# Kernel optimization log

Hardware: AMD Instinct MI355X
Metric: run time of the kernel (lower is better)

## Reference

```python
import jax, jax.numpy as jnp
import numpy as np

B, Q, E, NH, L, P = 8, 1024, 256, 8, 4, 4
DH = E // NH
SHAPES = np.array([[128, 128], [64, 64], [32, 32], [16, 16]], dtype=np.int64)
STARTS = np.concatenate([[0], np.cumsum(SHAPES.prod(1))[:-1]]).astype(np.int64)
S_TOTAL = int(SHAPES.prod(1).sum())
EPS = 1e-5


def setup_inputs() -> dict:
    key = jax.random.key(0)
    ks = iter(jax.random.split(key, 40))
    def rn(shp, s=0.02):
        return jax.random.normal(next(ks), shp, jnp.float32) * s
    return {
        "tgt": rn((B, Q, E), 1.0),
        "query_pos": rn((B, Q, E), 1.0),
        "reference_points": jax.random.uniform(next(ks), (B, Q, L, 2), jnp.float32),
        "src": rn((B, S_TOTAL, E), 1.0),
        "spatial_shapes": jnp.asarray(SHAPES),
        "level_start_index": jnp.asarray(STARTS),
        "in_proj_w": rn((3 * E, E)), "in_proj_b": jnp.zeros((3 * E,), jnp.float32),
        "out_proj_w": rn((E, E)), "out_proj_b": jnp.zeros((E,), jnp.float32),
        "norm1_g": jnp.ones((E,), jnp.float32), "norm1_b": jnp.zeros((E,), jnp.float32),
        "off_w": rn((NH * L * P * 2, E)), "off_b": rn((NH * L * P * 2,), 0.5),
        "aw_w": rn((NH * L * P, E)), "aw_b": jnp.zeros((NH * L * P,), jnp.float32),
        "vp_w": rn((E, E)), "vp_b": jnp.zeros((E,), jnp.float32),
        "op_w": rn((E, E)), "op_b": jnp.zeros((E,), jnp.float32),
        "norm2_g": jnp.ones((E,), jnp.float32), "norm2_b": jnp.zeros((E,), jnp.float32),
        "w1": rn((4 * E, E)), "b1": jnp.zeros((4 * E,), jnp.float32),
        "w2": rn((E, 4 * E)), "b2": jnp.zeros((E,), jnp.float32),
        "norm3_g": jnp.ones((E,), jnp.float32), "norm3_b": jnp.zeros((E,), jnp.float32),
    }


def _ln(x, g, b):
    mu = x.mean(-1, keepdims=True)
    var = ((x - mu) ** 2).mean(-1, keepdims=True)
    return (x - mu) * jax.lax.rsqrt(var + EPS) * g + b


def _bilinear(v, loc, Hl, Wl):
    # v: [B,NH,S_l,DH], loc in [0,1]: [B,NH,Q,P,2] -> [B,NH,Q,P,DH]
    # matches torch grid_sample(align_corners=False, padding='zeros')
    x = loc[..., 0] * Wl - 0.5
    y = loc[..., 1] * Hl - 0.5
    x0 = jnp.floor(x)
    y0 = jnp.floor(y)
    wx = (x - x0)[..., None]
    wy = (y - y0)[..., None]
    def g(yi, xi):
        valid = ((xi >= 0) & (xi <= Wl - 1) & (yi >= 0) & (yi <= Hl - 1)).astype(v.dtype)
        idx = (jnp.clip(yi, 0, Hl - 1) * Wl + jnp.clip(xi, 0, Wl - 1)).astype(jnp.int32)
        out = jnp.take_along_axis(v, idx.reshape(B, NH, Q * P, 1), axis=2)
        return out.reshape(B, NH, Q, P, DH) * valid[..., None]
    v00 = g(y0, x0); v01 = g(y0, x0 + 1.0)
    v10 = g(y0 + 1.0, x0); v11 = g(y0 + 1.0, x0 + 1.0)
    return (v00 * (1 - wy) * (1 - wx) + v01 * (1 - wy) * wx
            + v10 * wy * (1 - wx) + v11 * wy * wx)


def _forward(tgt, query_pos, reference_points, src,
             in_proj_w, in_proj_b, out_proj_w, out_proj_b, norm1_g, norm1_b,
             off_w, off_b, aw_w, aw_b, vp_w, vp_b, op_w, op_b,
             norm2_g, norm2_b, w1, b1, w2, b2, norm3_g, norm3_b,
             spatial_shapes, level_start_index):
    shp = np.asarray(spatial_shapes)
    starts = np.asarray(level_start_index)
    # ---- self-attention (q = k = tgt + pos, v = tgt) ----
    qk = tgt + query_pos
    wq, wk, wv = jnp.split(in_proj_w, 3, axis=0)
    bq, bk, bv = jnp.split(in_proj_b, 3, axis=0)
    q = (qk @ wq.T + bq).reshape(B, Q, NH, DH)
    k = (qk @ wk.T + bk).reshape(B, Q, NH, DH)
    v = (tgt @ wv.T + bv).reshape(B, Q, NH, DH)
    scores = jnp.einsum("bqhd,bkhd->bhqk", q, k) / jnp.sqrt(jnp.float32(DH))
    attn = jax.nn.softmax(scores, axis=-1)
    ctx = jnp.einsum("bhqk,bkhd->bqhd", attn, v).reshape(B, Q, E)
    tgt = _ln(tgt + (ctx @ out_proj_w.T + out_proj_b), norm1_g, norm1_b)
    # ---- MSDA cross-attention ----
    query = tgt + query_pos
    value = (src @ vp_w.T + vp_b).reshape(B, S_TOTAL, NH, DH).transpose(0, 2, 1, 3)  # [B,NH,S,DH]
    off = (query @ off_w.T + off_b).reshape(B, Q, NH, L, P, 2)
    aw = jax.nn.softmax((query @ aw_w.T + aw_b).reshape(B, Q, NH, L * P), -1)
    aw = aw.reshape(B, Q, NH, L, P)
    normalizer = jnp.asarray(shp[:, ::-1].copy(), jnp.float32)  # [L,2] = (W,H)
    loc = reference_points[:, :, None, :, None, :] + off / normalizer[None, None, None, :, None, :]
    loc = jnp.transpose(loc, (0, 2, 1, 3, 4, 5))  # [B,NH,Q,L,P,2]
    awt = jnp.transpose(aw, (0, 2, 1, 3, 4))      # [B,NH,Q,L,P]
    out = jnp.zeros((B, NH, Q, DH), jnp.float32)
    for l in range(L):
        Hl, Wl = int(shp[l, 0]), int(shp[l, 1])
        s0 = int(starts[l])
        vl = value[:, :, s0:s0 + Hl * Wl]
        samp = _bilinear(vl, loc[:, :, :, l], Hl, Wl)         # [B,NH,Q,P,DH]
        out = out + (samp * awt[:, :, :, l, :, None]).sum(3)
    ca = out.transpose(0, 2, 1, 3).reshape(B, Q, E) @ op_w.T + op_b
    tgt = _ln(tgt + ca, norm2_g, norm2_b)
    # ---- FFN ----
    h = jax.nn.relu(tgt @ w1.T + b1) @ w2.T + b2
    return _ln(tgt + h, norm3_g, norm3_b)


def reference(tgt, query_pos, reference_points, src, spatial_shapes, level_start_index,
              in_proj_w, in_proj_b, out_proj_w, out_proj_b, norm1_g, norm1_b,
              off_w, off_b, aw_w, aw_b, vp_w, vp_b, op_w, op_b,
              norm2_g, norm2_b, w1, b1, w2, b2, norm3_g, norm3_b):
    return _forward(tgt, query_pos, reference_points, src,
                    in_proj_w, in_proj_b, out_proj_w, out_proj_b, norm1_g, norm1_b,
                    off_w, off_b, aw_w, aw_b, vp_w, vp_b, op_w, op_b,
                    norm2_g, norm2_b, w1, b1, w2, b2, norm3_g, norm3_b,
                    spatial_shapes, level_start_index)
```

## Files before the change

kernel.cpp:

```cpp
#include <hip/hip_runtime.h>
#include <hip/hip_bf16.h>
#include <math.h>

typedef __hip_bfloat16 bf16;
typedef unsigned short ushort_t;

#define BQ 8
#define QLEN 1024
#define EMB 256
#define NHD 8
#define NLVL 4
#define NPT 4
#define DHD 32
#define STOT 21760

typedef short s8v __attribute__((ext_vector_type(8)));
typedef float f4v __attribute__((ext_vector_type(4)));

__device__ __forceinline__ float b2f(bf16 x) { return __bfloat162float(x); }

__device__ __forceinline__ float ldin(const void* p, int bf, size_t i) {
    return bf ? __bfloat162float(((const bf16*)p)[i]) : ((const float*)p)[i];
}

__device__ __forceinline__ float bfraw(unsigned u) {
    union { unsigned i; float f; } c; c.i = u << 16; return c.f;
}

__device__ __forceinline__ unsigned short f2us(float x) {
    bf16 h = __float2bfloat16(x);
    unsigned short u;
    __builtin_memcpy(&u, &h, 2);
    return u;
}

__global__ void detect_dtype(const unsigned* __restrict__ n1g, int* __restrict__ flag) {
    if (threadIdx.x == 0) flag[0] = (n1g[0] == 0x3F800000u) ? 0 : 1;
}

template <bool ARAW, bool RELU, typename CT>
__global__ __launch_bounds__(256) void gemm_mfma(const void* __restrict__ A,
                                                 const void* __restrict__ W, int w0,
                                                 const void* __restrict__ bias, int b0,
                                                 CT* __restrict__ C,
                                                 int M, int N, int K,
                                                 const int* __restrict__ dflag) {
    const int bfm = *dflag;
    __shared__ ushort_t As[128][40];
    __shared__ ushort_t Bs[128][40];
    const int tid = threadIdx.x;
    const int lane = tid & 63;
    const int wv = tid >> 6;
    const int wrow = (wv & 1) << 6;
    const int wcol = (wv >> 1) << 6;
    const int m0 = blockIdx.x * 128, n0 = blockIdx.y * 128;
    const int l15 = lane & 15, lhi = lane >> 4;

    f4v acc[4][4] = {};

    for (int k0 = 0; k0 < K; k0 += 32) {
        __syncthreads();
#pragma unroll
        for (int i = 0; i < 2; ++i) {
            const int idx = tid + 256 * i;
            const int r = idx >> 2, c = (idx & 3) << 3;
            const size_t aoff = (size_t)(m0 + r) * K + k0 + c;
            if (!ARAW || bfm) {
                *(uint4*)&As[r][c] = *(const uint4*)((const ushort_t*)A + aoff);
            } else {
                const float* af = (const float*)A + aoff;
                const float4 f0 = *(const float4*)af;
                const float4 f1 = *(const float4*)(af + 4);
                ushort_t t[8] = {f2us(f0.x), f2us(f0.y), f2us(f0.z), f2us(f0.w),
                                 f2us(f1.x), f2us(f1.y), f2us(f1.z), f2us(f1.w)};
                *(uint4*)&As[r][c] = *(uint4*)t;
            }
            const size_t woff = (size_t)(w0 + n0 + r) * K + k0 + c;
            if (bfm) {
                *(uint4*)&Bs[r][c] = *(const uint4*)((const ushort_t*)W + woff);
            } else {
                const float* wf = (const float*)W + woff;
                const float4 f0 = *(const float4*)wf;
                const float4 f1 = *(const float4*)(wf + 4);
                ushort_t t[8] = {f2us(f0.x), f2us(f0.y), f2us(f0.z), f2us(f0.w),
                                 f2us(f1.x), f2us(f1.y), f2us(f1.z), f2us(f1.w)};
                *(uint4*)&Bs[r][c] = *(uint4*)t;
            }
        }
        __syncthreads();

        s8v afr[4], bfr[4];
#pragma unroll
        for (int i = 0; i < 4; ++i)
            afr[i] = *(const s8v*)&As[wrow + i * 16 + l15][lhi * 8];
#pragma unroll
        for (int j = 0; j < 4; ++j)
            bfr[j] = *(const s8v*)&Bs[wcol + j * 16 + l15][lhi * 8];
#pragma unroll
        for (int i = 0; i < 4; ++i)
#pragma unroll
            for (int j = 0; j < 4; ++j)
                acc[i][j] = __builtin_amdgcn_mfma_f32_16x16x32_bf16(
                    afr[i], bfr[j], acc[i][j], 0, 0, 0);
    }

#pragma unroll
    for (int j = 0; j < 4; ++j) {
        const int n = n0 + wcol + j * 16 + l15;
        const float bv = ldin(bias, bfm, b0 + n);
#pragma unroll
        for (int i = 0; i < 4; ++i) {
#pragma unroll
            for (int p = 0; p < 4; ++p) {
                const int m = m0 + wrow + i * 16 + lhi * 4 + p;
                float v = acc[i][j][p] + bv;
                if (RELU) v = fmaxf(v, 0.f);
                if (sizeof(CT) == 2) ((ushort_t*)C)[(size_t)m * N + n] = f2us(v);
                else                 ((float*)C)[(size_t)m * N + n] = v;
            }
        }
    }
}

__global__ void ew_add_bf(const void* __restrict__ a, const void* __restrict__ b,
                          ushort_t* __restrict__ c, int n, const int* __restrict__ dflag) {
    const int bfm = *dflag;
    int i = blockIdx.x * 256 + threadIdx.x;
    if (i < n) c[i] = f2us(ldin(a, bfm, i) + ldin(b, bfm, i));
}

__global__ __launch_bounds__(256) void attn_mfma(const ushort_t* __restrict__ qkbuf,
                                                 const ushort_t* __restrict__ v,
                                                 ushort_t* __restrict__ ctx) {
    __shared__ ushort_t Ks[64][40];
    __shared__ ushort_t Vt[32][72];
    __shared__ ushort_t Ps[4][16][72];
    const int bh = blockIdx.y;
    const int b = bh >> 3, h = bh & 7;
    const int qt = blockIdx.x;
    const int tid = threadIdx.x;
    const int lane = tid & 63;
    const int wv = tid >> 6;
    const int l15 = lane & 15, quad = lane >> 4;
    const float scale = 0.17677669529663689f;

    const int qbase = (qt << 6) + (wv << 4);
    const s8v qfrag = *(const s8v*)(qkbuf +
        ((size_t)(b * QLEN + qbase + l15)) * 512 + h * DHD + quad * 8);

    const int sk = tid >> 2;
    const int sd = (tid & 3) << 3;

    float m_run[4] = {-1e30f, -1e30f, -1e30f, -1e30f};
    float l_run[4] = {};
    f4v o[2] = {};

    for (int kt = 0; kt < 16; ++kt) {
        __syncthreads();
        const size_t krow = (size_t)(b * QLEN + (kt << 6) + sk);
        *(uint4*)&Ks[sk][sd] = *(const uint4*)(qkbuf + krow * 512 + 256 + h * DHD + sd);
        const uint4 uv = *(const uint4*)(v + krow * 256 + h * DHD + sd);
        ushort_t vt[8];
        *(uint4*)vt = uv;
#pragma unroll
        for (int j = 0; j < 8; ++j) Vt[sd + j][sk] = vt[j];
        __syncthreads();

        f4v s4[4];
#pragma unroll
        for (int kb = 0; kb < 4; ++kb) {
            const s8v kfr = *(const s8v*)&Ks[(kb << 4) + l15][quad * 8];
            s4[kb] = __builtin_amdgcn_mfma_f32_16x16x32_bf16(qfrag, kfr, f4v{}, 0, 0, 0);
        }

        float sc[4][4];
#pragma unroll
        for (int kb = 0; kb < 4; ++kb)
#pragma unroll
            for (int p = 0; p < 4; ++p) sc[kb][p] = s4[kb][p] * scale;
        float mp[4];
#pragma unroll
        for (int p = 0; p < 4; ++p)
            mp[p] = fmaxf(fmaxf(sc[0][p], sc[1][p]), fmaxf(sc[2][p], sc[3][p]));
#pragma unroll
        for (int p = 0; p < 4; ++p) {
            mp[p] = fmaxf(mp[p], __shfl_xor(mp[p], 1, 64));
            mp[p] = fmaxf(mp[p], __shfl_xor(mp[p], 2, 64));
            mp[p] = fmaxf(mp[p], __shfl_xor(mp[p], 4, 64));
            mp[p] = fmaxf(mp[p], __shfl_xor(mp[p], 8, 64));
        }
        float al[4], ls[4] = {};
#pragma unroll
        for (int p = 0; p < 4; ++p) {
            const float mn = fmaxf(m_run[p], mp[p]);
            al[p] = __expf(m_run[p] - mn);
            m_run[p] = mn;
        }
        float pe[4][4];
#pragma unroll
        for (int kb = 0; kb < 4; ++kb)
#pragma unroll
            for (int p = 0; p < 4; ++p) {
                const float e = __expf(sc[kb][p] - m_run[p]);
                pe[kb][p] = e;
                ls[p] += e;
            }
#pragma unroll
        for (int p = 0; p < 4; ++p) {
            ls[p] += __shfl_xor(ls[p], 1, 64);
            ls[p] += __shfl_xor(ls[p], 2, 64);
            ls[p] += __shfl_xor(ls[p], 4, 64);
            ls[p] += __shfl_xor(ls[p], 8, 64);
            l_run[p] = l_run[p] * al[p] + ls[p];
        }
#pragma unroll
        for (int nb = 0; nb < 2; ++nb)
#pragma unroll
            for (int p = 0; p < 4; ++p) o[nb][p] *= al[p];

#pragma unroll
        for (int kb = 0; kb < 4; ++kb)
#pragma unroll
            for (int p = 0; p < 4; ++p)
                Ps[wv][(quad << 2) + p][(kb << 4) + l15] = f2us(pe[kb][p]);

#pragma unroll
        for (int kk = 0; kk < 2; ++kk) {
            const s8v afr = *(const s8v*)&Ps[wv][l15][kk * 32 + quad * 8];
#pragma unroll
            for (int nb = 0; nb < 2; ++nb) {
                const s8v bfr = *(const s8v*)&Vt[nb * 16 + l15][kk * 32 + quad * 8];
                o[nb] = __builtin_amdgcn_mfma_f32_16x16x32_bf16(afr, bfr, o[nb], 0, 0, 0);
            }
        }
    }

#pragma unroll
    for (int p = 0; p < 4; ++p) {
        const float inv = 1.f / l_run[p];
        const size_t row = (size_t)(b * QLEN + qbase + (quad << 2) + p) * EMB + h * DHD;
#pragma unroll
        for (int nb = 0; nb < 2; ++nb)
            ctx[row + nb * 16 + l15] = f2us(o[nb][p] * inv);
    }
}

__global__ __launch_bounds__(256) void ln_kernel(const void* __restrict__ xb,
                                                 const float* __restrict__ xf1,
                                                 const float* __restrict__ xf2,
                                                 const void* __restrict__ g,
                                                 const void* __restrict__ bta,
                                                 float* __restrict__ out_f,
                                                 ushort_t* __restrict__ out_b,
                                                 void* __restrict__ out_d,
                                                 const void* __restrict__ qp,
                                                 ushort_t* __restrict__ out_q,
                                                 const int* __restrict__ dflag) {
    const int bf = *dflag;
    const int row = blockIdx.x, t = threadIdx.x;
    const size_t base = (size_t)row * EMB + t;
    float x = 0.f;
    if (xb) x += ldin(xb, bf, base);
    if (xf1) x += xf1[base];
    if (xf2) x += xf2[base];
    __shared__ float red[256];
    red[t] = x;
    __syncthreads();
    for (int o = 128; o > 0; o >>= 1) { if (t < o) red[t] += red[t + o]; __syncthreads(); }
    const float mu = red[0] * (1.f / EMB);
    __syncthreads();
    const float dx = x - mu;
    red[t] = dx * dx;
    __syncthreads();
    for (int o = 128; o > 0; o >>= 1) { if (t < o) red[t] += red[t + o]; __syncthreads(); }
    const float var = red[0] * (1.f / EMB);
    const float y = dx * rsqrtf(var + 1e-5f) * ldin(g, bf, t) + ldin(bta, bf, t);
    if (out_f) out_f[base] = y;
    if (out_b) out_b[base] = f2us(y);
    if (out_d) {
        if (bf) ((ushort_t*)out_d)[base] = f2us(y);
        else    ((float*)out_d)[base] = y;
    }
    if (out_q) out_q[base] = f2us(y + ldin(qp, bf, base));
}

__global__ __launch_bounds__(64) void sample_kernel(const float* __restrict__ offb,
                                                    const float* __restrict__ awb,
                                                    const void* __restrict__ refp,
                                                    const ushort_t* __restrict__ value,
                                                    ushort_t* __restrict__ out,
                                                    const int* __restrict__ dflag) {
    const int bf = *dflag;
    const int bid = blockIdx.x;
    const int h = bid & 7;
    const int bq = bid >> 3;
    const int b = bq >> 10;
    const int lane = threadIdx.x;
    const int s_idx = lane >> 2;
    const int dg = lane & 3;
    const int l = s_idx >> 2;

    float logit = awb[(size_t)bq * 128 + h * 16 + s_idx];
    float m = logit;
#pragma unroll
    for (int o = 32; o > 0; o >>= 1) m = fmaxf(m, __shfl_xor(m, o, 64));
    float e = __expf(logit - m);
    float ssum = e;
#pragma unroll
    for (int o = 32; o > 0; o >>= 1) ssum += __shfl_xor(ssum, o, 64);
    const float paw = 4.f * e / ssum;

    const int Wi = 128 >> l;
    const float Wl = (float)Wi, Hl = (float)Wi;
    const int s0 = (l == 0) ? 0 : (l == 1) ? 16384 : (l == 2) ? 20480 : 21504;

    const float rx = ldin(refp, bf, ((size_t)bq * NLVL + l) * 2 + 0);
    const float ry = ldin(refp, bf, ((size_t)bq * NLVL + l) * 2 + 1);
    const float ox = offb[(size_t)bq * 256 + h * 32 + s_idx * 2 + 0];
    const float oy = offb[(size_t)bq * 256 + h * 32 + s_idx * 2 + 1];
    const float x = (rx + ox / Wl) * Wl - 0.5f;
    const float y = (ry + oy / Hl) * Hl - 0.5f;
    const float x0 = floorf(x), y0 = floorf(y);
    const float wx = x - x0, wy = y - y0;

    float acc[8] = {};
    const ushort_t* vbase = value + ((size_t)b * STOT) * EMB + h * DHD + dg * 8;

    auto corner = [&](float yi, float xi, float w) {
        const bool valid = (xi >= 0.f) && (xi <= Wl - 1.f) && (yi >= 0.f) && (yi <= Hl - 1.f);
        const float xc = fminf(fmaxf(xi, 0.f), Wl - 1.f);
        const float yc = fminf(fmaxf(yi, 0.f), Hl - 1.f);
        const int row = s0 + (int)yc * Wi + (int)xc;
        const uint4 u = *(const uint4*)(vbase + (size_t)row * EMB);
        const float wv = valid ? w : 0.f;
        const unsigned ua[4] = {u.x, u.y, u.z, u.w};
#pragma unroll
        for (int j = 0; j < 4; ++j) {
            acc[2 * j + 0] = fmaf(wv, bfraw(ua[j] & 0xffffu), acc[2 * j + 0]);
            acc[2 * j + 1] = fmaf(wv, bfraw(ua[j] >> 16), acc[2 * j + 1]);
        }
    };
    corner(y0, x0, (1.f - wy) * (1.f - wx));
    corner(y0, x0 + 1.f, (1.f - wy) * wx);
    corner(y0 + 1.f, x0, wy * (1.f - wx));
    corner(y0 + 1.f, x0 + 1.f, wy * wx);

#pragma unroll
    for (int j = 0; j < 8; ++j) {
        float vj = acc[j] * paw;
        vj += __shfl_xor(vj, 4, 64);
        vj += __shfl_xor(vj, 8, 64);
        vj += __shfl_xor(vj, 16, 64);
        vj += __shfl_xor(vj, 32, 64);
        acc[j] = vj;
    }
    if (s_idx == 0) {
        ushort_t t[8];
#pragma unroll
        for (int j = 0; j < 8; ++j) t[j] = f2us(acc[j]);
        *(uint4*)(out + (size_t)bq * EMB + h * DHD + dg * 8) = *(uint4*)t;
    }
}

extern "C" void kernel_launch(void* const* d_in, const int* in_sizes, int n_in,
                              void* d_out, int out_size, void* d_ws, size_t ws_size,
                              hipStream_t stream) {
    const void* tgt  = d_in[0];
    const void* qp   = d_in[1];
    const void* refp = d_in[2];
    const void* src  = d_in[3];
    const void* ipw  = d_in[6];
    const void* ipb  = d_in[7];
    const void* oprw = d_in[8];
    const void* oprb = d_in[9];
    const void* n1g  = d_in[10];
    const void* n1b  = d_in[11];
    const void* ofw  = d_in[12];
    const void* ofb  = d_in[13];
    const void* aww  = d_in[14];
    const void* awbv = d_in[15];
    const void* vpw  = d_in[16];
    const void* vpb  = d_in[17];
    const void* opw2 = d_in[18];
    const void* opb2 = d_in[19];
    const void* n2g  = d_in[20];
    const void* n2b  = d_in[21];
    const void* w1   = d_in[22];
    const void* b1   = d_in[23];
    const void* w2   = d_in[24];
    const void* b2   = d_in[25];
    const void* n3g  = d_in[26];
    const void* n3b  = d_in[27];

    const int M = BQ * QLEN;
    const int MS = BQ * STOT;

    char* ws = (char*)d_ws;
    int* dflag = (int*)ws;
    size_t o = 256;
    char* S1 = ws + o; o += (size_t)M * EMB * 2;
    char* S2 = ws + o; o += (size_t)M * 512 * 2;
    char* S3 = ws + o; o += (size_t)M * EMB * 2;
    char* S4 = ws + o; o += (size_t)M * EMB * 2;
    char* S5 = ws + o; o += (size_t)M * EMB * 4;
    char* S6 = ws + o; o += (size_t)M * EMB * 4;
    char* S7 = ws + o; o += (size_t)M * EMB * 4;
    char* S8 = ws + o;

    ushort_t* qk_bf    = (ushort_t*)S1;
    ushort_t* samp_bf  = (ushort_t*)S1;
    ushort_t* qkproj   = (ushort_t*)S2;
    float*    off_f    = (float*)S2;
    ushort_t* vproj    = (ushort_t*)S3;
    ushort_t* qry_bf   = (ushort_t*)S3;
    ushort_t* tgt2_bf  = (ushort_t*)S3;
    ushort_t* ctx_bf   = (ushort_t*)S4;
    float*    awl_f    = (float*)S4;
    float*    bufD     = (float*)S5;
    float*    tgt1_f   = (float*)S6;
    float*    tgt2_f   = (float*)S7;
    ushort_t* value_bf = (ushort_t*)S8;
    ushort_t* h1_bf    = (ushort_t*)S8;

    detect_dtype<<<1, 64, 0, stream>>>((const unsigned*)n1g, dflag);

    ew_add_bf<<<(M * EMB) / 256, 256, 0, stream>>>(tgt, qp, qk_bf, M * EMB, dflag);
    gemm_mfma<false, false, ushort_t><<<dim3(M / 128, 4), 256, 0, stream>>>(
        qk_bf, ipw, 0, ipb, 0, qkproj, M, 512, 256, dflag);
    gemm_mfma<true, false, ushort_t><<<dim3(M / 128, 2), 256, 0, stream>>>(
        tgt, ipw, 512, ipb, 512, vproj, M, 256, 256, dflag);
    attn_mfma<<<dim3(16, BQ * NHD), 256, 0, stream>>>(qkproj, vproj, ctx_bf);
    gemm_mfma<false, false, float><<<dim3(M / 128, 2), 256, 0, stream>>>(
        ctx_bf, oprw, 0, oprb, 0, bufD, M, 256, 256, dflag);
    ln_kernel<<<M, 256, 0, stream>>>(tgt, bufD, nullptr, n1g, n1b,
                                     tgt1_f, nullptr, nullptr, qp, qry_bf, dflag);

    gemm_mfma<false, false, float><<<dim3(M / 128, 2), 256, 0, stream>>>(
        qry_bf, ofw, 0, ofb, 0, off_f, M, 256, 256, dflag);
    gemm_mfma<false, false, float><<<dim3(M / 128, 1), 256, 0, stream>>>(
        qry_bf, aww, 0, awbv, 0, awl_f, M, 128, 256, dflag);
    gemm_mfma<true, false, ushort_t><<<dim3(MS / 128, 2), 256, 0, stream>>>(
        src, vpw, 0, vpb, 0, value_bf, MS, 256, 256, dflag);
    sample_kernel<<<M * NHD, 64, 0, stream>>>(off_f, awl_f, refp, value_bf, samp_bf, dflag);
    gemm_mfma<false, false, float><<<dim3(M / 128, 2), 256, 0, stream>>>(
        samp_bf, opw2, 0, opb2, 0, bufD, M, 256, 256, dflag);
    ln_kernel<<<M, 256, 0, stream>>>(nullptr, tgt1_f, bufD, n2g, n2b,
                                     tgt2_f, tgt2_bf, nullptr, nullptr, nullptr, dflag);

    gemm_mfma<false, true, ushort_t><<<dim3(M / 128, 8), 256, 0, stream>>>(
        tgt2_bf, w1, 0, b1, 0, h1_bf, M, 1024, 256, dflag);
    gemm_mfma<false, false, float><<<dim3(M / 128, 2), 256, 0, stream>>>(
        h1_bf, w2, 0, b2, 0, bufD, M, 256, 1024, dflag);
    ln_kernel<<<M, 256, 0, stream>>>(nullptr, tgt2_f, bufD, n3g, n3b,
                                     nullptr, nullptr, d_out, nullptr, nullptr, dflag);
}
```

Baseline: 701.5 us.

## Prefetch GEMM tiles into registers and parametrize block tile shape per call

The MFMA GEMM now loads the next K-slice from global memory into registers while the current slice is being computed from shared memory, then stores it to LDS at the top of the next iteration. The kernel is templated on the wave grid (WR x WC). Most small-M GEMMs now use 64x128 tiles with 128 threads to launch more blocks, and the large value projection uses a 128x256 tile with 512 threads. This hides global load latency and improves CU fill for the M=8192 GEMMs, at the cost of more registers per thread and an extra barrier per iteration.

```diff
diff --git a/kernel.cpp b/kernel.cpp
--- a/kernel.cpp
+++ b/kernel.cpp
@@ -38,56 +38,94 @@
     if (threadIdx.x == 0) flag[0] = (n1g[0] == 0x3F800000u) ? 0 : 1;
 }
 
-template <bool ARAW, bool RELU, typename CT>
-__global__ __launch_bounds__(256) void gemm_mfma(const void* __restrict__ A,
-                                                 const void* __restrict__ W, int w0,
-                                                 const void* __restrict__ bias, int b0,
-                                                 CT* __restrict__ C,
-                                                 int M, int N, int K,
-                                                 const int* __restrict__ dflag) {
+template <bool ARAW, bool RELU, typename CT, int WR, int WC>
+__global__ __launch_bounds__(64 * WR * WC) void gemm_mfma(
+        const void* __restrict__ A,
+        const void* __restrict__ W, int w0,
+        const void* __restrict__ bias, int b0,
+        CT* __restrict__ C,
+        int M, int N, int K,
+        const int* __restrict__ dflag) {
+    constexpr int T = 64 * WR * WC;
+    constexpr int BM = 64 * WR, BN = 64 * WC;
+    constexpr int AI = (BM * 4) / T;
+    constexpr int BI = (BN * 4) / T;
     const int bfm = *dflag;
-    __shared__ ushort_t As[128][40];
-    __shared__ ushort_t Bs[128][40];
+    __shared__ ushort_t As[BM][40];
+    __shared__ ushort_t Bs[BN][40];
     const int tid = threadIdx.x;
     const int lane = tid & 63;
     const int wv = tid >> 6;
-    const int wrow = (wv & 1) << 6;
-    const int wcol = (wv >> 1) << 6;
-    const int m0 = blockIdx.x * 128, n0 = blockIdx.y * 128;
+    const int wrow = (wv % WR) << 6;
+    const int wcol = (wv / WR) << 6;
+    const int m0 = blockIdx.x * BM, n0 = blockIdx.y * BN;
     const int l15 = lane & 15, lhi = lane >> 4;
 
     f4v acc[4][4] = {};
 
-    for (int k0 = 0; k0 < K; k0 += 32) {
-        __syncthreads();
-#pragma unroll
-        for (int i = 0; i < 2; ++i) {
-            const int idx = tid + 256 * i;
+    uint4 ra[AI], rb[BI];
+    float4 fa[AI][2], fb[BI][2];
+
+    auto ld = [&](int k0) {
+#pragma unroll
+        for (int i = 0; i < AI; ++i) {
+            const int idx = tid + T * i;
             const int r = idx >> 2, c = (idx & 3) << 3;
             const size_t aoff = (size_t)(m0 + r) * K + k0 + c;
             if (!ARAW || bfm) {
-                *(uint4*)&As[r][c] = *(const uint4*)((const ushort_t*)A + aoff);
+                ra[i] = *(const uint4*)((const ushort_t*)A + aoff);
             } else {
                 const float* af = (const float*)A + aoff;
-                const float4 f0 = *(const float4*)af;
-                const float4 f1 = *(const float4*)(af + 4);
-                ushort_t t[8] = {f2us(f0.x), f2us(f0.y), f2us(f0.z), f2us(f0.w),
-                                 f2us(f1.x), f2us(f1.y), f2us(f1.z), f2us(f1.w)};
-                *(uint4*)&As[r][c] = *(uint4*)t;
-            }
+                fa[i][0] = *(const float4*)af;
+                fa[i][1] = *(const float4*)(af + 4);
+            }
+        }
+#pragma unroll
+        for (int i = 0; i < BI; ++i) {
+            const int idx = tid + T * i;
+            const int r = idx >> 2, c = (idx & 3) << 3;
             const size_t woff = (size_t)(w0 + n0 + r) * K + k0 + c;
             if (bfm) {
-                *(uint4*)&Bs[r][c] = *(const uint4*)((const ushort_t*)W + woff);
+                rb[i] = *(const uint4*)((const ushort_t*)W + woff);
             } else {
                 const float* wf = (const float*)W + woff;
-                const float4 f0 = *(const float4*)wf;
-                const float4 f1 = *(const float4*)(wf + 4);
-                ushort_t t[8] = {f2us(f0.x), f2us(f0.y), f2us(f0.z), f2us(f0.w),
-                                 f2us(f1.x), f2us(f1.y), f2us(f1.z), f2us(f1.w)};
+                fb[i][0] = *(const float4*)wf;
+                fb[i][1] = *(const float4*)(wf + 4);
+            }
+        }
+    };
+    auto st = [&]() {
+#pragma unroll
+        for (int i = 0; i < AI; ++i) {
+            const int idx = tid + T * i;
+            const int r = idx >> 2, c = (idx & 3) << 3;
+            if (!ARAW || bfm) {
+                *(uint4*)&As[r][c] = ra[i];
+            } else {
+                ushort_t t[8] = {f2us(fa[i][0].x), f2us(fa[i][0].y), f2us(fa[i][0].z), f2us(fa[i][0].w),
+                                 f2us(fa[i][1].x), f2us(fa[i][1].y), f2us(fa[i][1].z), f2us(fa[i][1].w)};
+                *(uint4*)&As[r][c] = *(uint4*)t;
+            }
+        }
+#pragma unroll
+        for (int i = 0; i < BI; ++i) {
+            const int idx = tid + T * i;
+            const int r = idx >> 2, c = (idx & 3) << 3;
+            if (bfm) {
+                *(uint4*)&Bs[r][c] = rb[i];
+            } else {
+                ushort_t t[8] = {f2us(fb[i][0].x), f2us(fb[i][0].y), f2us(fb[i][0].z), f2us(fb[i][0].w),
+                                 f2us(fb[i][1].x), f2us(fb[i][1].y), f2us(fb[i][1].z), f2us(fb[i][1].w)};
                 *(uint4*)&Bs[r][c] = *(uint4*)t;
             }
         }
+    };
+
+    ld(0);
+    for (int k0 = 0; k0 < K; k0 += 32) {
+        st();
         __syncthreads();
+        if (k0 + 32 < K) ld(k0 + 32);
 
         s8v afr[4], bfr[4];
 #pragma unroll
@@ -102,6 +140,7 @@
             for (int j = 0; j < 4; ++j)
                 acc[i][j] = __builtin_amdgcn_mfma_f32_16x16x32_bf16(
                     afr[i], bfr[j], acc[i][j], 0, 0, 0);
+        __syncthreads();
     }
 
 #pragma unroll
@@ -425,31 +464,31 @@
     detect_dtype<<<1, 64, 0, stream>>>((const unsigned*)n1g, dflag);
 
     ew_add_bf<<<(M * EMB) / 256, 256, 0, stream>>>(tgt, qp, qk_bf, M * EMB, dflag);
-    gemm_mfma<false, false, ushort_t><<<dim3(M / 128, 4), 256, 0, stream>>>(
+    gemm_mfma<false, false, ushort_t, 1, 2><<<dim3(M / 64, 4), 128, 0, stream>>>(
         qk_bf, ipw, 0, ipb, 0, qkproj, M, 512, 256, dflag);
-    gemm_mfma<true, false, ushort_t><<<dim3(M / 128, 2), 256, 0, stream>>>(
+    gemm_mfma<true, false, ushort_t, 1, 2><<<dim3(M / 64, 2), 128, 0, stream>>>(
         tgt, ipw, 512, ipb, 512, vproj, M, 256, 256, dflag);
     attn_mfma<<<dim3(16, BQ * NHD), 256, 0, stream>>>(qkproj, vproj, ctx_bf);
-    gemm_mfma<false, false, float><<<dim3(M / 128, 2), 256, 0, stream>>>(
+    gemm_mfma<false, false, float, 1, 2><<<dim3(M / 64, 2), 128, 0, stream>>>(
         ctx_bf, oprw, 0, oprb, 0, bufD, M, 256, 256, dflag);
     ln_kernel<<<M, 256, 0, stream>>>(tgt, bufD, nullptr, n1g, n1b,
                                      tgt1_f, nullptr, nullptr, qp, qry_bf, dflag);
 
-    gemm_mfma<false, false, float><<<dim3(M / 128, 2), 256, 0, stream>>>(
+    gemm_mfma<false, false, float, 1, 2><<<dim3(M / 64, 2), 128, 0, stream>>>(
         qry_bf, ofw, 0, ofb, 0, off_f, M, 256, 256, dflag);
-    gemm_mfma<false, false, float><<<dim3(M / 128, 1), 256, 0, stream>>>(
+    gemm_mfma<false, false, float, 1, 2><<<dim3(M / 64, 1), 128, 0, stream>>>(
         qry_bf, aww, 0, awbv, 0, awl_f, M, 128, 256, dflag);
-    gemm_mfma<true, false, ushort_t><<<dim3(MS / 128, 2), 256, 0, stream>>>(
+    gemm_mfma<true, false, ushort_t, 2, 4><<<dim3(MS / 128, 1), 512, 0, stream>>>(
         src, vpw, 0, vpb, 0, value_bf, MS, 256, 256, dflag);
     sample_kernel<<<M * NHD, 64, 0, stream>>>(off_f, awl_f, refp, value_bf, samp_bf, dflag);
-    gemm_mfma<false, false, float><<<dim3(M / 128, 2), 256, 0, stream>>>(
+    gemm_mfma<false, false, float, 1, 2><<<dim3(M / 64, 2), 128, 0, stream>>>(
         samp_bf, opw2, 0, opb2, 0, bufD, M, 256, 256, dflag);
     ln_kernel<<<M, 256, 0, stream>>>(nullptr, tgt1_f, bufD, n2g, n2b,
                                      tgt2_f, tgt2_bf, nullptr, nullptr, nullptr, dflag);
 
-    gemm_mfma<false, true, ushort_t><<<dim3(M / 128, 8), 256, 0, stream>>>(
+    gemm_mfma<false, true, ushort_t, 1, 2><<<dim3(M / 64, 8), 128, 0, stream>>>(
         tgt2_bf, w1, 0, b1, 0, h1_bf, M, 1024, 256, dflag);
-    gemm_mfma<false, false, float><<<dim3(M / 128, 2), 256, 0, stream>>>(
+    gemm_mfma<false, false, float, 1, 2><<<dim3(M / 64, 2), 128, 0, stream>>>(
         h1_bf, w2, 0, b2, 0, bufD, M, 256, 1024, dflag);
     ln_kernel<<<M, 256, 0, stream>>>(nullptr, tgt2_f, bufD, n3g, n3b,
                                      nullptr, nullptr, d_out, nullptr, nullptr, dflag);
```

New measurement: 697.3 us. Within noise of the previous version (-0.6%).
